# Kernel tuning notes

Measured on AMD Instinct MI355X. Metric: run time of the kernel, lower is better.

## Reference

```python
import jax, jax.numpy as jnp
import numpy as np

T, B, N, C = 4, 16, 256, 512
H = 8
HID = 4 * C
TAU = 2.0
EPS = 1e-5
SCALE = 0.125

@jax.custom_vjp
def spike_fn(x):
    return (x >= 0.0).astype(x.dtype)

def _spike_fwd(x):
    return spike_fn(x), x

def _spike_bwd(x, g):
    alpha = 4.0  # spikingjelly sigmoid surrogate default
    s = jax.nn.sigmoid(alpha * x)
    return (g * alpha * s * (1.0 - s),)

spike_fn.defvjp(_spike_fwd, _spike_bwd)

def lif(x_seq, v_th=1.0):
    # Multi-step LIF: v += (x - v)/tau (decay_input, v_reset=0), hard reset, detach_reset
    def step(v, xt):
        v = v + (xt - v) / TAU
        s = spike_fn(v - v_th)
        v = v * (1.0 - jax.lax.stop_gradient(s))
        return v, s
    _, out = jax.lax.scan(step, jnp.zeros_like(x_seq[0]), x_seq)
    return out

def lin_bn(x2d, w, b, g, beta):
    # Linear then BatchNorm1d (training mode, per-channel stats over all rows).
    # BN on (TB, Cout, N) over (batch, N) == BN on flattened (TB*N, Cout) over axis 0.
    y = x2d @ w.T + b
    mu = jnp.mean(y, axis=0)
    var = jnp.var(y, axis=0)
    return g * (y - mu) * jax.lax.rsqrt(var + EPS) + beta

def setup_inputs() -> dict:
    key = jax.random.key(0)
    ks = jax.random.split(key, 10)
    d = {
        "x": jax.random.normal(ks[0], (T, B, N, C), jnp.float32),
        "s_x": jax.random.normal(ks[1], (T, B, N, C), jnp.float32),
    }
    def lin(k, cout, cin):
        return jax.random.normal(k, (cout, cin), jnp.float32) * 0.02
    d["qw"] = lin(ks[2], C, C); d["qb"] = jnp.zeros((C,), jnp.float32)
    d["qg"] = jnp.ones((C,), jnp.float32); d["qbeta"] = jnp.zeros((C,), jnp.float32)
    d["kw"] = lin(ks[3], C, C); d["kb"] = jnp.zeros((C,), jnp.float32)
    d["kg"] = jnp.ones((C,), jnp.float32); d["kbeta"] = jnp.zeros((C,), jnp.float32)
    d["vw"] = lin(ks[4], C, C); d["vb"] = jnp.zeros((C,), jnp.float32)
    d["vg"] = jnp.ones((C,), jnp.float32); d["vbeta"] = jnp.zeros((C,), jnp.float32)
    d["pw"] = lin(ks[5], C, C); d["pb"] = jnp.zeros((C,), jnp.float32)
    d["pg"] = jnp.ones((C,), jnp.float32); d["pbeta"] = jnp.zeros((C,), jnp.float32)
    d["f1w"] = lin(ks[6], HID, C); d["f1b"] = jnp.zeros((HID,), jnp.float32)
    d["f1g"] = jnp.ones((HID,), jnp.float32); d["f1beta"] = jnp.zeros((HID,), jnp.float32)
    d["f2w"] = lin(ks[7], C, HID); d["f2b"] = jnp.zeros((C,), jnp.float32)
    d["f2g"] = jnp.ones((C,), jnp.float32); d["f2beta"] = jnp.zeros((C,), jnp.float32)
    return d

def _block(x, s_x, qw, qb, qg, qbeta, kw, kb, kg, kbeta, vw, vb, vg, vbeta,
           pw, pb, pg, pbeta, f1w, f1b, f1g, f1beta, f2w, f2b, f2g, f2beta):
    Dh = C // H
    xf = x.reshape(T * B * N, C)
    # SSA (s_x is unused in the source forward)
    q = lif(lin_bn(xf, qw, qb, qg, qbeta).reshape(T, B, N, C))
    k = lif(lin_bn(xf, kw, kb, kg, kbeta).reshape(T, B, N, C))
    v = lin_bn(xf, vw, vb, vg, vbeta).reshape(T, B, N, C)  # v has no LIF in source
    q = q.reshape(T, B, N, H, Dh).transpose(0, 1, 3, 2, 4)  # tbhnd
    k = k.reshape(T, B, N, H, Dh).transpose(0, 1, 3, 2, 4)
    v = v.reshape(T, B, N, H, Dh).transpose(0, 1, 3, 2, 4)
    attn = jnp.einsum('tbhnd,tbhmd->tbhnm', q, k) * SCALE  # no softmax
    o = jnp.einsum('tbhnm,tbhmd->tbhnd', attn, v)
    o = o.transpose(0, 1, 3, 2, 4).reshape(T * B * N, C)
    o = lin_bn(o, pw, pb, pg, pbeta).reshape(T, B, N, C)
    x = x + o
    # MLP
    xf2 = x.reshape(T * B * N, C)
    h = lif(lin_bn(xf2, f1w, f1b, f1g, f1beta).reshape(T, B, N, HID))
    m = lif(lin_bn(h.reshape(T * B * N, HID), f2w, f2b, f2g, f2beta).reshape(T, B, N, C))
    return x + m

def reference(x, s_x, qw, qb, qg, qbeta, kw, kb, kg, kbeta, vw, vb, vg, vbeta,
              pw, pb, pg, pbeta, f1w, f1b, f1g, f1beta, f2w, f2b, f2g, f2beta):
    return _block(x, s_x, qw, qb, qg, qbeta, kw, kb, kg, kbeta, vw, vb, vg, vbeta,
                  pw, pb, pg, pbeta, f1w, f1b, f1g, f1beta, f2w, f2b, f2g, f2beta)
```

## Files before the change

### kernel.cpp

```cpp
#include <hip/hip_runtime.h>
#include <cstdint>

#define T_ 4
#define B_ 16
#define N_ 256
#define C_ 512
#define H_ 8
#define HID_ 2048
#define M_ (T_*B_*N_)
#define BNP_ (B_*N_)

__global__ __launch_bounds__(256)
void gemm_nt(const float* __restrict__ A, const float* __restrict__ W,
             const float* __restrict__ bias, float* __restrict__ Y,
             int Nc, int K) {
  __shared__ float As[16][132];
  __shared__ float Ws[16][132];
  const int tid  = threadIdx.x;
  const int row0 = blockIdx.y * 128;
  const int col0 = blockIdx.x * 128;
  const int tx = tid & 15, ty = tid >> 4;

  float acc[8][8];
  #pragma unroll
  for (int i = 0; i < 8; ++i)
    #pragma unroll
    for (int j = 0; j < 8; ++j) acc[i][j] = 0.f;

  const int ar = tid >> 2;
  const int ac = (tid & 3) << 2;

  for (int k0 = 0; k0 < K; k0 += 16) {
    __syncthreads();
    #pragma unroll
    for (int i = 0; i < 2; ++i) {
      int r = ar + i * 64;
      float4 a4 = *(const float4*)(A + (size_t)(row0 + r) * K + (k0 + ac));
      As[ac+0][r] = a4.x; As[ac+1][r] = a4.y; As[ac+2][r] = a4.z; As[ac+3][r] = a4.w;
      float4 w4 = *(const float4*)(W + (size_t)(col0 + r) * K + (k0 + ac));
      Ws[ac+0][r] = w4.x; Ws[ac+1][r] = w4.y; Ws[ac+2][r] = w4.z; Ws[ac+3][r] = w4.w;
    }
    __syncthreads();
    #pragma unroll
    for (int kk = 0; kk < 16; ++kk) {
      float a[8], b[8];
      *(float4*)&a[0] = *(const float4*)&As[kk][ty*8];
      *(float4*)&a[4] = *(const float4*)&As[kk][ty*8+4];
      *(float4*)&b[0] = *(const float4*)&Ws[kk][tx*8];
      *(float4*)&b[4] = *(const float4*)&Ws[kk][tx*8+4];
      #pragma unroll
      for (int i = 0; i < 8; ++i)
        #pragma unroll
        for (int j = 0; j < 8; ++j)
          acc[i][j] = fmaf(a[i], b[j], acc[i][j]);
    }
  }
  #pragma unroll
  for (int i = 0; i < 8; ++i) {
    size_t r = (size_t)(row0 + ty*8 + i);
    #pragma unroll
    for (int j4 = 0; j4 < 2; ++j4) {
      int c = col0 + tx*8 + j4*4;
      float4 o4;
      o4.x = acc[i][j4*4+0] + bias[c+0];
      o4.y = acc[i][j4*4+1] + bias[c+1];
      o4.z = acc[i][j4*4+2] + bias[c+2];
      o4.w = acc[i][j4*4+3] + bias[c+3];
      *(float4*)(Y + r * Nc + c) = o4;
    }
  }
}

__global__ __launch_bounds__(256)
void gemm_nt_f64acc(const float* __restrict__ A, const float* __restrict__ W,
                    const float* __restrict__ bias, float* __restrict__ Y,
                    int Nc, int K) {
  __shared__ float As[16][68];
  __shared__ float Ws[16][68];
  const int tid  = threadIdx.x;
  const int row0 = blockIdx.y * 64;
  const int col0 = blockIdx.x * 64;
  const int tx = tid & 15, ty = tid >> 4;

  double acc[4][4];
  #pragma unroll
  for (int i = 0; i < 4; ++i)
    #pragma unroll
    for (int j = 0; j < 4; ++j) acc[i][j] = 0.0;

  const int lr = tid >> 2;
  const int lk = (tid & 3) << 2;

  for (int k0 = 0; k0 < K; k0 += 16) {
    __syncthreads();
    {
      float4 a4 = *(const float4*)(A + (size_t)(row0 + lr) * K + (k0 + lk));
      As[lk+0][lr] = a4.x; As[lk+1][lr] = a4.y; As[lk+2][lr] = a4.z; As[lk+3][lr] = a4.w;
      float4 w4 = *(const float4*)(W + (size_t)(col0 + lr) * K + (k0 + lk));
      Ws[lk+0][lr] = w4.x; Ws[lk+1][lr] = w4.y; Ws[lk+2][lr] = w4.z; Ws[lk+3][lr] = w4.w;
    }
    __syncthreads();
    #pragma unroll
    for (int kk = 0; kk < 16; ++kk) {
      double a[4], b[4];
      #pragma unroll
      for (int i = 0; i < 4; ++i) a[i] = (double)As[kk][ty*4+i];
      #pragma unroll
      for (int j = 0; j < 4; ++j) b[j] = (double)Ws[kk][tx*4+j];
      #pragma unroll
      for (int i = 0; i < 4; ++i)
        #pragma unroll
        for (int j = 0; j < 4; ++j)
          acc[i][j] = fma(a[i], b[j], acc[i][j]);
    }
  }
  #pragma unroll
  for (int i = 0; i < 4; ++i) {
    size_t r = (size_t)(row0 + ty*4 + i);
    int c = col0 + tx*4;
    float4 o4;
    o4.x = (float)(acc[i][0] + (double)bias[c+0]);
    o4.y = (float)(acc[i][1] + (double)bias[c+1]);
    o4.z = (float)(acc[i][2] + (double)bias[c+2]);
    o4.w = (float)(acc[i][3] + (double)bias[c+3]);
    *(float4*)(Y + r * Nc + c) = o4;
  }
}

__global__ __launch_bounds__(256)
void col_stats_partial(const float* __restrict__ Y, int Nc,
                       float* __restrict__ psum, float* __restrict__ psq) {
  const int r0 = blockIdx.x * 32;
  for (int c = threadIdx.x; c < Nc; c += 256) {
    float s = 0.f, q = 0.f;
    const float* p = Y + (size_t)r0 * Nc + c;
    for (int r = 0; r < 32; ++r) {
      float v = p[(size_t)r * Nc];
      s += v;
      q = fmaf(v, v, q);
    }
    psum[(size_t)blockIdx.x * Nc + c] = s;
    psq [(size_t)blockIdx.x * Nc + c] = q;
  }
}

__global__ void col_stats_final(const float* __restrict__ psum, const float* __restrict__ psq,
                                int Nc, const float* __restrict__ g, const float* __restrict__ beta,
                                float* __restrict__ chp) {
  int c = blockIdx.x * blockDim.x + threadIdx.x;
  if (c >= Nc) return;
  double s = 0.0, q = 0.0;
  for (int p = 0; p < 512; ++p) {
    s += (double)psum[(size_t)p * Nc + c];
    q += (double)psq [(size_t)p * Nc + c];
  }
  double mean = s / (double)M_;
  double var  = q / (double)M_ - mean * mean;
  float alpha = g[c] / sqrtf((float)var + 1e-5f);
  chp[2*c]   = alpha;
  chp[2*c+1] = fmaf(-(float)mean, alpha, beta[c]);
}

__global__ void col_stats_final_f64(const float* __restrict__ psum, const float* __restrict__ psq,
                                    int Nc, const float* __restrict__ g, const float* __restrict__ beta,
                                    double* __restrict__ chpd) {
  int c = blockIdx.x * blockDim.x + threadIdx.x;
  if (c >= Nc) return;
  double s = 0.0, q = 0.0;
  for (int p = 0; p < 512; ++p) {
    s += (double)psum[(size_t)p * Nc + c];
    q += (double)psq [(size_t)p * Nc + c];
  }
  double mean = s / (double)M_;
  double var  = q / (double)M_ - mean * mean;
  double alpha = (double)g[c] / sqrt(var + 1e-5);
  chpd[2*c]   = alpha;
  chpd[2*c+1] = (double)beta[c] - mean * alpha;
}

__global__ __launch_bounds__(256)
void bnlif_mask(const float* __restrict__ Y, const float* __restrict__ chp,
                unsigned long long* __restrict__ mask) {
  int lane = threadIdx.x & 63;
  int u  = blockIdx.x * 4 + (threadIdx.x >> 6);
  int bn = u >> 3, cg = u & 7;
  int c  = cg * 64 + lane;
  float alpha = chp[2*c], bb = chp[2*c+1];
  float v = 0.f;
  #pragma unroll
  for (int t = 0; t < 4; ++t) {
    float y  = Y[((size_t)(t * BNP_ + bn)) * C_ + c];
    float uu = fmaf(y, alpha, bb);
    v = v + (uu - v) * 0.5f;
    bool sp = (v >= 1.0f);
    unsigned long long m = __ballot(sp);
    if (sp) v = 0.f;
    if (lane == 0) mask[((size_t)(t * BNP_ + bn)) * H_ + cg] = m;
  }
}

__global__ void bn_apply_f64(const float* __restrict__ Y, const double* __restrict__ chpd,
                             float* __restrict__ out) {
  const long total4 = (long)M_ * C_ / 4;
  for (long i = (long)blockIdx.x * blockDim.x + threadIdx.x; i < total4;
       i += (long)gridDim.x * blockDim.x) {
    int c4 = (int)(i & (C_/4 - 1)) * 4;
    float4 y = ((const float4*)Y)[i];
    float4 r;
    r.x = (float)fma((double)y.x, chpd[2*(c4+0)], chpd[2*(c4+0)+1]);
    r.y = (float)fma((double)y.y, chpd[2*(c4+1)], chpd[2*(c4+1)+1]);
    r.z = (float)fma((double)y.z, chpd[2*(c4+2)], chpd[2*(c4+2)+1]);
    r.w = (float)fma((double)y.w, chpd[2*(c4+3)], chpd[2*(c4+3)+1]);
    ((float4*)out)[i] = r;
  }
}

__global__ void bn_residual_f64(const float* __restrict__ Y, const double* __restrict__ chpd,
                                const float* __restrict__ x, float* __restrict__ out) {
  const long total4 = (long)M_ * C_ / 4;
  for (long i = (long)blockIdx.x * blockDim.x + threadIdx.x; i < total4;
       i += (long)gridDim.x * blockDim.x) {
    int c4 = (int)(i & (C_/4 - 1)) * 4;
    float4 y = ((const float4*)Y)[i];
    float4 xv = ((const float4*)x)[i];
    float4 r;
    r.x = (float)((double)xv.x + fma((double)y.x, chpd[2*(c4+0)], chpd[2*(c4+0)+1]));
    r.y = (float)((double)xv.y + fma((double)y.y, chpd[2*(c4+1)], chpd[2*(c4+1)+1]));
    r.z = (float)((double)xv.z + fma((double)y.z, chpd[2*(c4+2)], chpd[2*(c4+2)+1]));
    r.w = (float)((double)xv.w + fma((double)y.w, chpd[2*(c4+3)], chpd[2*(c4+3)+1]));
    ((float4*)out)[i] = r;
  }
}

__global__ __launch_bounds__(256)
void bnlif_inplace(float* __restrict__ Y, const float* __restrict__ chp) {
  int c  = blockIdx.x * 256 + threadIdx.x;
  int bn = blockIdx.y;
  float alpha = chp[2*c], bb = chp[2*c+1];
  float v = 0.f;
  #pragma unroll
  for (int t = 0; t < 4; ++t) {
    size_t idx = ((size_t)(t * BNP_ + bn)) * HID_ + c;
    float uu = fmaf(Y[idx], alpha, bb);
    v = v + (uu - v) * 0.5f;
    bool sp = (v >= 1.f);
    Y[idx] = sp ? 1.f : 0.f;
    if (sp) v = 0.f;
  }
}

__global__ __launch_bounds__(256)
void bnlif_final(const float* __restrict__ Y, const float* __restrict__ chp,
                 const float* __restrict__ xo, float* __restrict__ out) {
  int c  = blockIdx.x * 256 + threadIdx.x;
  int bn = blockIdx.y;
  float alpha = chp[2*c], bb = chp[2*c+1];
  float v = 0.f;
  #pragma unroll
  for (int t = 0; t < 4; ++t) {
    size_t idx = ((size_t)(t * BNP_ + bn)) * C_ + c;
    float uu = fmaf(Y[idx], alpha, bb);
    v = v + (uu - v) * 0.5f;
    bool sp = (v >= 1.f);
    out[idx] = xo[idx] + (sp ? 1.f : 0.f);
    if (sp) v = 0.f;
  }
}

__global__ __launch_bounds__(256)
void attn_kernel_f64(const unsigned long long* __restrict__ qmask,
                     const unsigned long long* __restrict__ kmask,
                     const float* __restrict__ v, float* __restrict__ o) {
  __shared__ unsigned long long km[256];
  __shared__ float vt[256][64];
  int rb  = blockIdx.x & 3;
  int tbh = blockIdx.x >> 2;
  int h   = tbh & 7, tb = tbh >> 3;
  int tid = threadIdx.x;

  km[tid] = kmask[(size_t)(tb * 256 + tid) * H_ + h];
  const float* vbase = v + (size_t)tb * 256 * C_ + h * 64;
  #pragma unroll
  for (int i = 0; i < 16; ++i) {
    int f = i * 256 + tid;
    int r = f >> 4, c4 = f & 15;
    *(float4*)&vt[r][c4 * 4] = *(const float4*)(vbase + (size_t)r * C_ + c4 * 4);
  }
  int lane = tid & 63, w = tid >> 6;
  int nr = lane & 15, dg = lane >> 4;
  int n  = rb * 64 + w * 16 + nr;
  unsigned long long qm = qmask[(size_t)(tb * 256 + n) * H_ + h];
  __syncthreads();

  double acc[16];
  #pragma unroll
  for (int j = 0; j < 16; ++j) acc[j] = 0.0;

  for (int m = 0; m < 256; ++m) {
    double s = (double)__popcll(qm & km[m]) * 0.125;
    #pragma unroll
    for (int j = 0; j < 4; ++j) {
      float4 vv = *(const float4*)&vt[m][dg * 16 + j * 4];
      acc[j*4+0] = fma(s, (double)vv.x, acc[j*4+0]);
      acc[j*4+1] = fma(s, (double)vv.y, acc[j*4+1]);
      acc[j*4+2] = fma(s, (double)vv.z, acc[j*4+2]);
      acc[j*4+3] = fma(s, (double)vv.w, acc[j*4+3]);
    }
  }
  float* orow = o + (size_t)(tb * 256 + n) * C_ + h * 64 + dg * 16;
  #pragma unroll
  for (int j = 0; j < 4; ++j)
    *(float4*)(orow + j * 4) = make_float4((float)acc[j*4], (float)acc[j*4+1],
                                           (float)acc[j*4+2], (float)acc[j*4+3]);
}

extern "C" void kernel_launch(void* const* d_in, const int* in_sizes, int n_in,
                              void* d_out, int out_size, void* d_ws, size_t ws_size,
                              hipStream_t stream) {
  const float* x    = (const float*)d_in[0];
  const float* qw   = (const float*)d_in[2];
  const float* qb   = (const float*)d_in[3];
  const float* qg   = (const float*)d_in[4];
  const float* qbe  = (const float*)d_in[5];
  const float* kw   = (const float*)d_in[6];
  const float* kb   = (const float*)d_in[7];
  const float* kg   = (const float*)d_in[8];
  const float* kbe  = (const float*)d_in[9];
  const float* vw   = (const float*)d_in[10];
  const float* vb   = (const float*)d_in[11];
  const float* vg   = (const float*)d_in[12];
  const float* vbe  = (const float*)d_in[13];
  const float* pw   = (const float*)d_in[14];
  const float* pb   = (const float*)d_in[15];
  const float* pg   = (const float*)d_in[16];
  const float* pbe  = (const float*)d_in[17];
  const float* f1w  = (const float*)d_in[18];
  const float* f1b  = (const float*)d_in[19];
  const float* f1g  = (const float*)d_in[20];
  const float* f1be = (const float*)d_in[21];
  const float* f2w  = (const float*)d_in[22];
  const float* f2b  = (const float*)d_in[23];
  const float* f2g  = (const float*)d_in[24];
  const float* f2be = (const float*)d_in[25];

  char* ws = (char*)d_ws;
  float* bufY = (float*)(ws);
  float* bufV = (float*)(ws + 134217728ull);
  float* bufO = (float*)(ws + 167772160ull);
  unsigned long long* qmask = (unsigned long long*)(ws + 201326592ull);
  unsigned long long* kmask = (unsigned long long*)(ws + 202375168ull);
  float* psum = (float*)(ws + 203423744ull);
  float* psq  = (float*)(ws + 207618048ull);
  float* chp  = (float*)(ws + 211812352ull);
  double* chpd = (double*)(ws + 211828736ull);

  float* out = (float*)d_out;

  gemm_nt<<<dim3(4,128), 256, 0, stream>>>(x, qw, qb, bufY, C_, C_);
  col_stats_partial<<<512, 256, 0, stream>>>(bufY, C_, psum, psq);
  col_stats_final<<<2, 256, 0, stream>>>(psum, psq, C_, qg, qbe, chp);
  bnlif_mask<<<8192, 256, 0, stream>>>(bufY, chp, qmask);
  gemm_nt<<<dim3(4,128), 256, 0, stream>>>(x, kw, kb, bufY, C_, C_);
  col_stats_partial<<<512, 256, 0, stream>>>(bufY, C_, psum, psq);
  col_stats_final<<<2, 256, 0, stream>>>(psum, psq, C_, kg, kbe, chp);
  bnlif_mask<<<8192, 256, 0, stream>>>(bufY, chp, kmask);
  gemm_nt_f64acc<<<dim3(8,256), 256, 0, stream>>>(x, vw, vb, bufY, C_, C_);
  col_stats_partial<<<512, 256, 0, stream>>>(bufY, C_, psum, psq);
  col_stats_final_f64<<<2, 256, 0, stream>>>(psum, psq, C_, vg, vbe, chpd);
  bn_apply_f64<<<2048, 256, 0, stream>>>(bufY, chpd, bufV);
  attn_kernel_f64<<<2048, 256, 0, stream>>>(qmask, kmask, bufV, bufO);
  gemm_nt_f64acc<<<dim3(8,256), 256, 0, stream>>>(bufO, pw, pb, bufY, C_, C_);
  col_stats_partial<<<512, 256, 0, stream>>>(bufY, C_, psum, psq);
  col_stats_final_f64<<<2, 256, 0, stream>>>(psum, psq, C_, pg, pbe, chpd);
  bn_residual_f64<<<2048, 256, 0, stream>>>(bufY, chpd, x, bufO);
  gemm_nt<<<dim3(16,128), 256, 0, stream>>>(bufO, f1w, f1b, bufY, HID_, C_);
  col_stats_partial<<<512, 256, 0, stream>>>(bufY, HID_, psum, psq);
  col_stats_final<<<8, 256, 0, stream>>>(psum, psq, HID_, f1g, f1be, chp);
  bnlif_inplace<<<dim3(8,4096), 256, 0, stream>>>(bufY, chp);
  gemm_nt<<<dim3(4,128), 256, 0, stream>>>(bufY, f2w, f2b, bufV, C_, HID_);
  col_stats_partial<<<512, 256, 0, stream>>>(bufV, C_, psum, psq);
  col_stats_final<<<2, 256, 0, stream>>>(psum, psq, C_, f2g, f2be, chp);
  bnlif_final<<<dim3(2,4096), 256, 0, stream>>>(bufV, chp, bufO, out);
}
```

Baseline: 1.969 ms.

## Double-buffer shared memory in fp32 GEMM and shrink tile to 128x64

```diff
diff --git a/kernel.cpp b/kernel.cpp
--- a/kernel.cpp
+++ b/kernel.cpp
@@ -11,63 +11,84 @@
 #define BNP_ (B_*N_)
 
 __global__ __launch_bounds__(256)
-void gemm_nt(const float* __restrict__ A, const float* __restrict__ W,
-             const float* __restrict__ bias, float* __restrict__ Y,
-             int Nc, int K) {
-  __shared__ float As[16][132];
-  __shared__ float Ws[16][132];
+void gemm_nt_v2(const float* __restrict__ A, const float* __restrict__ W,
+                const float* __restrict__ bias, float* __restrict__ Y,
+                int Nc, int K) {
+  __shared__ float As[2][16][132];
+  __shared__ float Ws[2][16][68];
   const int tid  = threadIdx.x;
   const int row0 = blockIdx.y * 128;
-  const int col0 = blockIdx.x * 128;
+  const int col0 = blockIdx.x * 64;
   const int tx = tid & 15, ty = tid >> 4;
-
-  float acc[8][8];
+  const int ar = tid >> 2;
+  const int ac = (tid & 3) << 2;
+
+  float acc[8][4];
   #pragma unroll
   for (int i = 0; i < 8; ++i)
     #pragma unroll
-    for (int j = 0; j < 8; ++j) acc[i][j] = 0.f;
-
-  const int ar = tid >> 2;
-  const int ac = (tid & 3) << 2;
-
+    for (int j = 0; j < 4; ++j) acc[i][j] = 0.f;
+
+  const float* Ap0 = A + (size_t)(row0 + ar) * K + ac;
+  const float* Ap1 = A + (size_t)(row0 + ar + 64) * K + ac;
+  const float* Wp  = W + (size_t)(col0 + ar) * K + ac;
+
+  float4 pa0 = *(const float4*)(Ap0);
+  float4 pa1 = *(const float4*)(Ap1);
+  float4 pb  = *(const float4*)(Wp);
+
+  As[0][ac+0][ar] = pa0.x; As[0][ac+1][ar] = pa0.y;
+  As[0][ac+2][ar] = pa0.z; As[0][ac+3][ar] = pa0.w;
+  As[0][ac+0][ar+64] = pa1.x; As[0][ac+1][ar+64] = pa1.y;
+  As[0][ac+2][ar+64] = pa1.z; As[0][ac+3][ar+64] = pa1.w;
+  Ws[0][ac+0][ar] = pb.x; Ws[0][ac+1][ar] = pb.y;
+  Ws[0][ac+2][ar] = pb.z; Ws[0][ac+3][ar] = pb.w;
+  __syncthreads();
+
+  int buf = 0;
   for (int k0 = 0; k0 < K; k0 += 16) {
-    __syncthreads();
-    #pragma unroll
-    for (int i = 0; i < 2; ++i) {
-      int r = ar + i * 64;
-      float4 a4 = *(const float4*)(A + (size_t)(row0 + r) * K + (k0 + ac));
-      As[ac+0][r] = a4.x; As[ac+1][r] = a4.y; As[ac+2][r] = a4.z; As[ac+3][r] = a4.w;
-      float4 w4 = *(const float4*)(W + (size_t)(col0 + r) * K + (k0 + ac));
-      Ws[ac+0][r] = w4.x; Ws[ac+1][r] = w4.y; Ws[ac+2][r] = w4.z; Ws[ac+3][r] = w4.w;
-    }
-    __syncthreads();
+    const bool last = (k0 + 16 >= K);
+    if (!last) {
+      pa0 = *(const float4*)(Ap0 + k0 + 16);
+      pa1 = *(const float4*)(Ap1 + k0 + 16);
+      pb  = *(const float4*)(Wp  + k0 + 16);
+    }
     #pragma unroll
     for (int kk = 0; kk < 16; ++kk) {
-      float a[8], b[8];
-      *(float4*)&a[0] = *(const float4*)&As[kk][ty*8];
-      *(float4*)&a[4] = *(const float4*)&As[kk][ty*8+4];
-      *(float4*)&b[0] = *(const float4*)&Ws[kk][tx*8];
-      *(float4*)&b[4] = *(const float4*)&Ws[kk][tx*8+4];
+      float4 av0 = *(const float4*)&As[buf][kk][ty*8];
+      float4 av1 = *(const float4*)&As[buf][kk][ty*8+4];
+      float4 bv  = *(const float4*)&Ws[buf][kk][tx*4];
+      float a[8] = {av0.x, av0.y, av0.z, av0.w, av1.x, av1.y, av1.z, av1.w};
+      float b[4] = {bv.x, bv.y, bv.z, bv.w};
       #pragma unroll
       for (int i = 0; i < 8; ++i)
         #pragma unroll
-        for (int j = 0; j < 8; ++j)
+        for (int j = 0; j < 4; ++j)
           acc[i][j] = fmaf(a[i], b[j], acc[i][j]);
     }
-  }
+    if (!last) {
+      int nb = buf ^ 1;
+      As[nb][ac+0][ar] = pa0.x; As[nb][ac+1][ar] = pa0.y;
+      As[nb][ac+2][ar] = pa0.z; As[nb][ac+3][ar] = pa0.w;
+      As[nb][ac+0][ar+64] = pa1.x; As[nb][ac+1][ar+64] = pa1.y;
+      As[nb][ac+2][ar+64] = pa1.z; As[nb][ac+3][ar+64] = pa1.w;
+      Ws[nb][ac+0][ar] = pb.x; Ws[nb][ac+1][ar] = pb.y;
+      Ws[nb][ac+2][ar] = pb.z; Ws[nb][ac+3][ar] = pb.w;
+      __syncthreads();
+      buf = nb;
+    }
+  }
+
   #pragma unroll
   for (int i = 0; i < 8; ++i) {
     size_t r = (size_t)(row0 + ty*8 + i);
-    #pragma unroll
-    for (int j4 = 0; j4 < 2; ++j4) {
-      int c = col0 + tx*8 + j4*4;
-      float4 o4;
-      o4.x = acc[i][j4*4+0] + bias[c+0];
-      o4.y = acc[i][j4*4+1] + bias[c+1];
-      o4.z = acc[i][j4*4+2] + bias[c+2];
-      o4.w = acc[i][j4*4+3] + bias[c+3];
-      *(float4*)(Y + r * Nc + c) = o4;
-    }
+    int c = col0 + tx*4;
+    float4 o4;
+    o4.x = acc[i][0] + bias[c+0];
+    o4.y = acc[i][1] + bias[c+1];
+    o4.z = acc[i][2] + bias[c+2];
+    o4.w = acc[i][3] + bias[c+3];
+    *(float4*)(Y + r * Nc + c) = o4;
   }
 }
 
@@ -356,11 +377,11 @@
 
   float* out = (float*)d_out;
 
-  gemm_nt<<<dim3(4,128), 256, 0, stream>>>(x, qw, qb, bufY, C_, C_);
+  gemm_nt_v2<<<dim3(8,128), 256, 0, stream>>>(x, qw, qb, bufY, C_, C_);
   col_stats_partial<<<512, 256, 0, stream>>>(bufY, C_, psum, psq);
   col_stats_final<<<2, 256, 0, stream>>>(psum, psq, C_, qg, qbe, chp);
   bnlif_mask<<<8192, 256, 0, stream>>>(bufY, chp, qmask);
-  gemm_nt<<<dim3(4,128), 256, 0, stream>>>(x, kw, kb, bufY, C_, C_);
+  gemm_nt_v2<<<dim3(8,128), 256, 0, stream>>>(x, kw, kb, bufY, C_, C_);
   col_stats_partial<<<512, 256, 0, stream>>>(bufY, C_, psum, psq);
   col_stats_final<<<2, 256, 0, stream>>>(psum, psq, C_, kg, kbe, chp);
   bnlif_mask<<<8192, 256, 0, stream>>>(bufY, chp, kmask);
@@ -373,11 +394,11 @@
   col_stats_partial<<<512, 256, 0, stream>>>(bufY, C_, psum, psq);
   col_stats_final_f64<<<2, 256, 0, stream>>>(psum, psq, C_, pg, pbe, chpd);
   bn_residual_f64<<<2048, 256, 0, stream>>>(bufY, chpd, x, bufO);
-  gemm_nt<<<dim3(16,128), 256, 0, stream>>>(bufO, f1w, f1b, bufY, HID_, C_);
+  gemm_nt_v2<<<dim3(32,128), 256, 0, stream>>>(bufO, f1w, f1b, bufY, HID_, C_);
   col_stats_partial<<<512, 256, 0, stream>>>(bufY, HID_, psum, psq);
   col_stats_final<<<8, 256, 0, stream>>>(psum, psq, HID_, f1g, f1be, chp);
   bnlif_inplace<<<dim3(8,4096), 256, 0, stream>>>(bufY, chp);
-  gemm_nt<<<dim3(4,128), 256, 0, stream>>>(bufY, f2w, f2b, bufV, C_, HID_);
+  gemm_nt_v2<<<dim3(8,128), 256, 0, stream>>>(bufY, f2w, f2b, bufV, C_, HID_);
   col_stats_partial<<<512, 256, 0, stream>>>(bufV, C_, psum, psq);
   col_stats_final<<<2, 256, 0, stream>>>(psum, psq, C_, f2g, f2be, chp);
   bnlif_final<<<dim3(2,4096), 256, 0, stream>>>(bufV, chp, bufO, out);
```

Measured after the change: 2.000 ms. No clear change (+1.5%).

## Double-buffer GEMM shared tiles with register prefetch and add 64x128 tile variant

Applied to the files above, without the earlier changes.

```diff
diff --git a/kernel.cpp b/kernel.cpp
--- a/kernel.cpp
+++ b/kernel.cpp
@@ -10,51 +10,73 @@
 #define M_ (T_*B_*N_)
 #define BNP_ (B_*N_)
 
-__global__ __launch_bounds__(256)
-void gemm_nt(const float* __restrict__ A, const float* __restrict__ W,
-             const float* __restrict__ bias, float* __restrict__ Y,
-             int Nc, int K) {
-  __shared__ float As[16][132];
-  __shared__ float Ws[16][132];
+__global__ __launch_bounds__(256, 2)
+void gemm_f32_t128(const float* __restrict__ A, const float* __restrict__ W,
+                   const float* __restrict__ bias, float* __restrict__ Y,
+                   int Nc, int K) {
+  __shared__ float As[2][16][132];
+  __shared__ float Ws[2][16][132];
   const int tid  = threadIdx.x;
   const int row0 = blockIdx.y * 128;
   const int col0 = blockIdx.x * 128;
   const int tx = tid & 15, ty = tid >> 4;
-
-  float acc[8][8];
-  #pragma unroll
-  for (int i = 0; i < 8; ++i)
-    #pragma unroll
-    for (int j = 0; j < 8; ++j) acc[i][j] = 0.f;
-
   const int ar = tid >> 2;
   const int ac = (tid & 3) << 2;
 
+  float acc[8][8];
+  #pragma unroll
+  for (int i = 0; i < 8; ++i)
+    #pragma unroll
+    for (int j = 0; j < 8; ++j) acc[i][j] = 0.f;
+
+  const float* Ap0 = A + (size_t)(row0 + ar) * K + ac;
+  const float* Ap1 = A + (size_t)(row0 + ar + 64) * K + ac;
+  const float* Wp0 = W + (size_t)(col0 + ar) * K + ac;
+  const float* Wp1 = W + (size_t)(col0 + ar + 64) * K + ac;
+
+  float4 pa0 = *(const float4*)Ap0;
+  float4 pa1 = *(const float4*)Ap1;
+  float4 pw0 = *(const float4*)Wp0;
+  float4 pw1 = *(const float4*)Wp1;
+  As[0][ac+0][ar] = pa0.x; As[0][ac+1][ar] = pa0.y; As[0][ac+2][ar] = pa0.z; As[0][ac+3][ar] = pa0.w;
+  As[0][ac+0][ar+64] = pa1.x; As[0][ac+1][ar+64] = pa1.y; As[0][ac+2][ar+64] = pa1.z; As[0][ac+3][ar+64] = pa1.w;
+  Ws[0][ac+0][ar] = pw0.x; Ws[0][ac+1][ar] = pw0.y; Ws[0][ac+2][ar] = pw0.z; Ws[0][ac+3][ar] = pw0.w;
+  Ws[0][ac+0][ar+64] = pw1.x; Ws[0][ac+1][ar+64] = pw1.y; Ws[0][ac+2][ar+64] = pw1.z; Ws[0][ac+3][ar+64] = pw1.w;
+  __syncthreads();
+
+  int buf = 0;
   for (int k0 = 0; k0 < K; k0 += 16) {
-    __syncthreads();
-    #pragma unroll
-    for (int i = 0; i < 2; ++i) {
-      int r = ar + i * 64;
-      float4 a4 = *(const float4*)(A + (size_t)(row0 + r) * K + (k0 + ac));
-      As[ac+0][r] = a4.x; As[ac+1][r] = a4.y; As[ac+2][r] = a4.z; As[ac+3][r] = a4.w;
-      float4 w4 = *(const float4*)(W + (size_t)(col0 + r) * K + (k0 + ac));
-      Ws[ac+0][r] = w4.x; Ws[ac+1][r] = w4.y; Ws[ac+2][r] = w4.z; Ws[ac+3][r] = w4.w;
-    }
-    __syncthreads();
+    const bool last = (k0 + 16 >= K);
+    if (!last) {
+      pa0 = *(const float4*)(Ap0 + k0 + 16);
+      pa1 = *(const float4*)(Ap1 + k0 + 16);
+      pw0 = *(const float4*)(Wp0 + k0 + 16);
+      pw1 = *(const float4*)(Wp1 + k0 + 16);
+    }
     #pragma unroll
     for (int kk = 0; kk < 16; ++kk) {
       float a[8], b[8];
-      *(float4*)&a[0] = *(const float4*)&As[kk][ty*8];
-      *(float4*)&a[4] = *(const float4*)&As[kk][ty*8+4];
-      *(float4*)&b[0] = *(const float4*)&Ws[kk][tx*8];
-      *(float4*)&b[4] = *(const float4*)&Ws[kk][tx*8+4];
+      *(float4*)&a[0] = *(const float4*)&As[buf][kk][ty*8];
+      *(float4*)&a[4] = *(const float4*)&As[buf][kk][ty*8+4];
+      *(float4*)&b[0] = *(const float4*)&Ws[buf][kk][tx*8];
+      *(float4*)&b[4] = *(const float4*)&Ws[buf][kk][tx*8+4];
       #pragma unroll
       for (int i = 0; i < 8; ++i)
         #pragma unroll
         for (int j = 0; j < 8; ++j)
           acc[i][j] = fmaf(a[i], b[j], acc[i][j]);
     }
-  }
+    if (!last) {
+      int nb = buf ^ 1;
+      As[nb][ac+0][ar] = pa0.x; As[nb][ac+1][ar] = pa0.y; As[nb][ac+2][ar] = pa0.z; As[nb][ac+3][ar] = pa0.w;
+      As[nb][ac+0][ar+64] = pa1.x; As[nb][ac+1][ar+64] = pa1.y; As[nb][ac+2][ar+64] = pa1.z; As[nb][ac+3][ar+64] = pa1.w;
+      Ws[nb][ac+0][ar] = pw0.x; Ws[nb][ac+1][ar] = pw0.y; Ws[nb][ac+2][ar] = pw0.z; Ws[nb][ac+3][ar] = pw0.w;
+      Ws[nb][ac+0][ar+64] = pw1.x; Ws[nb][ac+1][ar+64] = pw1.y; Ws[nb][ac+2][ar+64] = pw1.z; Ws[nb][ac+3][ar+64] = pw1.w;
+      __syncthreads();
+      buf = nb;
+    }
+  }
+
   #pragma unroll
   for (int i = 0; i < 8; ++i) {
     size_t r = (size_t)(row0 + ty*8 + i);
@@ -72,48 +94,144 @@
 }
 
 __global__ __launch_bounds__(256)
-void gemm_nt_f64acc(const float* __restrict__ A, const float* __restrict__ W,
-                    const float* __restrict__ bias, float* __restrict__ Y,
-                    int Nc, int K) {
-  __shared__ float As[16][68];
-  __shared__ float Ws[16][68];
+void gemm_f32_t64x128(const float* __restrict__ A, const float* __restrict__ W,
+                      const float* __restrict__ bias, float* __restrict__ Y,
+                      int Nc, int K) {
+  __shared__ float As[2][16][68];
+  __shared__ float Ws[2][16][132];
+  const int tid  = threadIdx.x;
+  const int row0 = blockIdx.y * 64;
+  const int col0 = blockIdx.x * 128;
+  const int tx = tid & 15, ty = tid >> 4;
+  const int ar = tid >> 2;
+  const int ac = (tid & 3) << 2;
+
+  float acc[4][8];
+  #pragma unroll
+  for (int i = 0; i < 4; ++i)
+    #pragma unroll
+    for (int j = 0; j < 8; ++j) acc[i][j] = 0.f;
+
+  const float* Ap  = A + (size_t)(row0 + ar) * K + ac;
+  const float* Wp0 = W + (size_t)(col0 + ar) * K + ac;
+  const float* Wp1 = W + (size_t)(col0 + ar + 64) * K + ac;
+
+  float4 pa  = *(const float4*)Ap;
+  float4 pw0 = *(const float4*)Wp0;
+  float4 pw1 = *(const float4*)Wp1;
+  As[0][ac+0][ar] = pa.x; As[0][ac+1][ar] = pa.y; As[0][ac+2][ar] = pa.z; As[0][ac+3][ar] = pa.w;
+  Ws[0][ac+0][ar] = pw0.x; Ws[0][ac+1][ar] = pw0.y; Ws[0][ac+2][ar] = pw0.z; Ws[0][ac+3][ar] = pw0.w;
+  Ws[0][ac+0][ar+64] = pw1.x; Ws[0][ac+1][ar+64] = pw1.y; Ws[0][ac+2][ar+64] = pw1.z; Ws[0][ac+3][ar+64] = pw1.w;
+  __syncthreads();
+
+  int buf = 0;
+  for (int k0 = 0; k0 < K; k0 += 16) {
+    const bool last = (k0 + 16 >= K);
+    if (!last) {
+      pa  = *(const float4*)(Ap  + k0 + 16);
+      pw0 = *(const float4*)(Wp0 + k0 + 16);
+      pw1 = *(const float4*)(Wp1 + k0 + 16);
+    }
+    #pragma unroll
+    for (int kk = 0; kk < 16; ++kk) {
+      float4 av = *(const float4*)&As[buf][kk][ty*4];
+      float b[8];
+      *(float4*)&b[0] = *(const float4*)&Ws[buf][kk][tx*8];
+      *(float4*)&b[4] = *(const float4*)&Ws[buf][kk][tx*8+4];
+      float a[4] = {av.x, av.y, av.z, av.w};
+      #pragma unroll
+      for (int i = 0; i < 4; ++i)
+        #pragma unroll
+        for (int j = 0; j < 8; ++j)
+          acc[i][j] = fmaf(a[i], b[j], acc[i][j]);
+    }
+    if (!last) {
+      int nb = buf ^ 1;
+      As[nb][ac+0][ar] = pa.x; As[nb][ac+1][ar] = pa.y; As[nb][ac+2][ar] = pa.z; As[nb][ac+3][ar] = pa.w;
+      Ws[nb][ac+0][ar] = pw0.x; Ws[nb][ac+1][ar] = pw0.y; Ws[nb][ac+2][ar] = pw0.z; Ws[nb][ac+3][ar] = pw0.w;
+      Ws[nb][ac+0][ar+64] = pw1.x; Ws[nb][ac+1][ar+64] = pw1.y; Ws[nb][ac+2][ar+64] = pw1.z; Ws[nb][ac+3][ar+64] = pw1.w;
+      __syncthreads();
+      buf = nb;
+    }
+  }
+
+  #pragma unroll
+  for (int i = 0; i < 4; ++i) {
+    size_t r = (size_t)(row0 + ty*4 + i);
+    #pragma unroll
+    for (int j4 = 0; j4 < 2; ++j4) {
+      int c = col0 + tx*8 + j4*4;
+      float4 o4;
+      o4.x = acc[i][j4*4+0] + bias[c+0];
+      o4.y = acc[i][j4*4+1] + bias[c+1];
+      o4.z = acc[i][j4*4+2] + bias[c+2];
+      o4.w = acc[i][j4*4+3] + bias[c+3];
+      *(float4*)(Y + r * Nc + c) = o4;
+    }
+  }
+}
+
+__global__ __launch_bounds__(256)
+void gemm_f64_v2(const float* __restrict__ A, const float* __restrict__ W,
+                 const float* __restrict__ bias, float* __restrict__ Y,
+                 int Nc, int K) {
+  __shared__ double As[2][16][68];
+  __shared__ double Ws[2][16][68];
   const int tid  = threadIdx.x;
   const int row0 = blockIdx.y * 64;
   const int col0 = blockIdx.x * 64;
   const int tx = tid & 15, ty = tid >> 4;
-
-  double acc[4][4];
-  #pragma unroll
-  for (int i = 0; i < 4; ++i)
-    #pragma unroll
-    for (int j = 0; j < 4; ++j) acc[i][j] = 0.0;
-
   const int lr = tid >> 2;
   const int lk = (tid & 3) << 2;
 
+  double acc[4][4];
+  #pragma unroll
+  for (int i = 0; i < 4; ++i)
+    #pragma unroll
+    for (int j = 0; j < 4; ++j) acc[i][j] = 0.0;
+
+  const float* Ap = A + (size_t)(row0 + lr) * K + lk;
+  const float* Wp = W + (size_t)(col0 + lr) * K + lk;
+
+  float4 pa = *(const float4*)Ap;
+  float4 pw = *(const float4*)Wp;
+  As[0][lk+0][lr] = (double)pa.x; As[0][lk+1][lr] = (double)pa.y;
+  As[0][lk+2][lr] = (double)pa.z; As[0][lk+3][lr] = (double)pa.w;
+  Ws[0][lk+0][lr] = (double)pw.x; Ws[0][lk+1][lr] = (double)pw.y;
+  Ws[0][lk+2][lr] = (double)pw.z; Ws[0][lk+3][lr] = (double)pw.w;
+  __syncthreads();
+
+  int buf = 0;
   for (int k0 = 0; k0 < K; k0 += 16) {
-    __syncthreads();
-    {
-      float4 a4 = *(const float4*)(A + (size_t)(row0 + lr) * K + (k0 + lk));
-      As[lk+0][lr] = a4.x; As[lk+1][lr] = a4.y; As[lk+2][lr] = a4.z; As[lk+3][lr] = a4.w;
-      float4 w4 = *(const float4*)(W + (size_t)(col0 + lr) * K + (k0 + lk));
-      Ws[lk+0][lr] = w4.x; Ws[lk+1][lr] = w4.y; Ws[lk+2][lr] = w4.z; Ws[lk+3][lr] = w4.w;
-    }
-    __syncthreads();
+    const bool last = (k0 + 16 >= K);
+    if (!last) {
+      pa = *(const float4*)(Ap + k0 + 16);
+      pw = *(const float4*)(Wp + k0 + 16);
+    }
     #pragma unroll
     for (int kk = 0; kk < 16; ++kk) {
       double a[4], b[4];
-      #pragma unroll
-      for (int i = 0; i < 4; ++i) a[i] = (double)As[kk][ty*4+i];
-      #pragma unroll
-      for (int j = 0; j < 4; ++j) b[j] = (double)Ws[kk][tx*4+j];
+      *(double2*)&a[0] = *(const double2*)&As[buf][kk][ty*4];
+      *(double2*)&a[2] = *(const double2*)&As[buf][kk][ty*4+2];
+      *(double2*)&b[0] = *(const double2*)&Ws[buf][kk][tx*4];
+      *(double2*)&b[2] = *(const double2*)&Ws[buf][kk][tx*4+2];
       #pragma unroll
       for (int i = 0; i < 4; ++i)
         #pragma unroll
         for (int j = 0; j < 4; ++j)
           acc[i][j] = fma(a[i], b[j], acc[i][j]);
     }
-  }
+    if (!last) {
+      int nb = buf ^ 1;
+      As[nb][lk+0][lr] = (double)pa.x; As[nb][lk+1][lr] = (double)pa.y;
+      As[nb][lk+2][lr] = (double)pa.z; As[nb][lk+3][lr] = (double)pa.w;
+      Ws[nb][lk+0][lr] = (double)pw.x; Ws[nb][lk+1][lr] = (double)pw.y;
+      Ws[nb][lk+2][lr] = (double)pw.z; Ws[nb][lk+3][lr] = (double)pw.w;
+      __syncthreads();
+      buf = nb;
+    }
+  }
+
   #pragma unroll
   for (int i = 0; i < 4; ++i) {
     size_t r = (size_t)(row0 + ty*4 + i);
@@ -356,28 +474,28 @@
 
   float* out = (float*)d_out;
 
-  gemm_nt<<<dim3(4,128), 256, 0, stream>>>(x, qw, qb, bufY, C_, C_);
+  gemm_f32_t64x128<<<dim3(4,256), 256, 0, stream>>>(x, qw, qb, bufY, C_, C_);
   col_stats_partial<<<512, 256, 0, stream>>>(bufY, C_, psum, psq);
   col_stats_final<<<2, 256, 0, stream>>>(psum, psq, C_, qg, qbe, chp);
   bnlif_mask<<<8192, 256, 0, stream>>>(bufY, chp, qmask);
-  gemm_nt<<<dim3(4,128), 256, 0, stream>>>(x, kw, kb, bufY, C_, C_);
+  gemm_f32_t64x128<<<dim3(4,256), 256, 0, stream>>>(x, kw, kb, bufY, C_, C_);
   col_stats_partial<<<512, 256, 0, stream>>>(bufY, C_, psum, psq);
   col_stats_final<<<2, 256, 0, stream>>>(psum, psq, C_, kg, kbe, chp);
   bnlif_mask<<<8192, 256, 0, stream>>>(bufY, chp, kmask);
-  gemm_nt_f64acc<<<dim3(8,256), 256, 0, stream>>>(x, vw, vb, bufY, C_, C_);
+  gemm_f64_v2<<<dim3(8,256), 256, 0, stream>>>(x, vw, vb, bufY, C_, C_);
   col_stats_partial<<<512, 256, 0, stream>>>(bufY, C_, psum, psq);
   col_stats_final_f64<<<2, 256, 0, stream>>>(psum, psq, C_, vg, vbe, chpd);
   bn_apply_f64<<<2048, 256, 0, stream>>>(bufY, chpd, bufV);
   attn_kernel_f64<<<2048, 256, 0, stream>>>(qmask, kmask, bufV, bufO);
-  gemm_nt_f64acc<<<dim3(8,256), 256, 0, stream>>>(bufO, pw, pb, bufY, C_, C_);
+  gemm_f64_v2<<<dim3(8,256), 256, 0, stream>>>(bufO, pw, pb, bufY, C_, C_);
   col_stats_partial<<<512, 256, 0, stream>>>(bufY, C_, psum, psq);
   col_stats_final_f64<<<2, 256, 0, stream>>>(psum, psq, C_, pg, pbe, chpd);
   bn_residual_f64<<<2048, 256, 0, stream>>>(bufY, chpd, x, bufO);
-  gemm_nt<<<dim3(16,128), 256, 0, stream>>>(bufO, f1w, f1b, bufY, HID_, C_);
+  gemm_f32_t128<<<dim3(16,128), 256, 0, stream>>>(bufO, f1w, f1b, bufY, HID_, C_);
   col_stats_partial<<<512, 256, 0, stream>>>(bufY, HID_, psum, psq);
   col_stats_final<<<8, 256, 0, stream>>>(psum, psq, HID_, f1g, f1be, chp);
   bnlif_inplace<<<dim3(8,4096), 256, 0, stream>>>(bufY, chp);
-  gemm_nt<<<dim3(4,128), 256, 0, stream>>>(bufY, f2w, f2b, bufV, C_, HID_);
+  gemm_f32_t64x128<<<dim3(4,256), 256, 0, stream>>>(bufY, f2w, f2b, bufV, C_, HID_);
   col_stats_partial<<<512, 256, 0, stream>>>(bufV, C_, psum, psq);
   col_stats_final<<<2, 256, 0, stream>>>(psum, psq, C_, f2g, f2be, chp);
   bnlif_final<<<dim3(2,4096), 256, 0, stream>>>(bufV, chp, bufO, out);
```

Result: slower. 2.077 ms (+5.5%).
